# Performance work log

Hardware: AMD Instinct MI355X
Metric: run time of the kernel (lower is better)

Reference implementation:

```python
import jax, jax.numpy as jnp
import numpy as np

EPS = 0.05
T = 0.1
SINKHORN_ITERS = 3


def _l2norm(x, axis=1, eps=1e-12):
    # torch.nn.functional.normalize: x / max(||x||, eps)
    n = jnp.sqrt(jnp.sum(x * x, axis=axis, keepdims=True))
    return x / jnp.maximum(n, eps)


def _sinkhorn(sim, eps, niters):
    # SwAV-style sinkhorn. sim: [B, K]
    Q = jnp.exp(sim / eps).T            # [K, B]
    Q = Q / jnp.sum(Q)
    K, B = Q.shape

    def body(Qc, _):
        Qc = Qc / (jnp.sum(Qc, axis=1, keepdims=True) * K)  # row normalize
        Qc = Qc / (jnp.sum(Qc, axis=0, keepdims=True) * B)  # col normalize
        return Qc, None

    Q, _ = jax.lax.scan(body, Q, None, length=niters)
    return (Q * B).T                     # [B, K]


def _kl_div_logit(pred, target):
    # KLDivLoss(batchmean) on log_softmax(pred) vs target probs
    logp = jax.nn.log_softmax(pred, axis=1)
    B = pred.shape[0]
    return jnp.sum(target * (jnp.log(target) - logp)) / B


def _forward_once(c, nq, nk):
    sim = jnp.matmul(nk, c.T)                                 # [B, K]
    code = jax.lax.stop_gradient(_sinkhorn(sim, EPS, SINKHORN_ITERS))
    pred = jnp.matmul(nq, c.T) / T
    return _kl_div_logit(pred, code)


def setup_inputs() -> dict:
    key = jax.random.key(0)
    k1, k2, k3 = jax.random.split(key, 3)
    q = jax.random.normal(k1, (16384, 256), dtype=jnp.float32)
    k = jax.random.normal(k2, (16384, 256), dtype=jnp.float32)
    cluster_center = jax.random.normal(k3, (3000, 256), dtype=jnp.float32)
    return {"q": q, "k": k, "cluster_center": cluster_center}


def reference(q, k, cluster_center):
    nq = _l2norm(q, axis=1)
    nk = _l2norm(k, axis=1)
    c = _l2norm(cluster_center, axis=1)
    loss1 = _forward_once(c, nq, nk)
    loss2 = _forward_once(c, nk, nq)
    return (loss1 + loss2) / 2.0
```

## Files before the change

kernel.cpp:

```cpp
#include <hip/hip_runtime.h>

#define BATCH 16384
#define DIM   256
#define KC    3000
#define KCPAD 3072
#define NBLK  256

typedef __bf16   bf16x8  __attribute__((ext_vector_type(8)));
typedef float    floatx4 __attribute__((ext_vector_type(4)));
typedef _Float16 half8   __attribute__((ext_vector_type(8)));

#define GLD16(gptr, lptr)                                                              \
  __builtin_amdgcn_global_load_lds((const __attribute__((address_space(1))) void*)(gptr), \
                                   (__attribute__((address_space(3))) void*)(lptr), 16, 0, 0)

__device__ __forceinline__ float dpp_red_sum(float x) {
  int xi;
  xi = __builtin_amdgcn_update_dpp(0, __float_as_int(x), 0x111, 0xf, 0xf, true);
  x += __int_as_float(xi);
  xi = __builtin_amdgcn_update_dpp(0, __float_as_int(x), 0x112, 0xf, 0xf, true);
  x += __int_as_float(xi);
  xi = __builtin_amdgcn_update_dpp(0, __float_as_int(x), 0x114, 0xf, 0xf, true);
  x += __int_as_float(xi);
  xi = __builtin_amdgcn_update_dpp(0, __float_as_int(x), 0x118, 0xf, 0xf, true);
  x += __int_as_float(xi);
  xi = __builtin_amdgcn_update_dpp(0, __float_as_int(x), 0x142, 0xa, 0xf, false);
  x += __int_as_float(xi);
  xi = __builtin_amdgcn_update_dpp(0, __float_as_int(x), 0x143, 0xc, 0xf, false);
  x += __int_as_float(xi);
  return x;
}

__global__ __launch_bounds__(256) void normalize_all(const float* __restrict__ q,
                                                     const float* __restrict__ k,
                                                     const float* __restrict__ c,
                                                     __bf16* __restrict__ nq,
                                                     __bf16* __restrict__ nk,
                                                     __bf16* __restrict__ nc) {
  __shared__ float s4[4];
  int row = blockIdx.x;
  int t = threadIdx.x;
  const float* src;
  __bf16* dst;
  int srow;
  bool live;
  if (row < BATCH) {
    src = q; dst = nq; srow = row; live = true;
  } else if (row < 2 * BATCH) {
    src = k; dst = nk; srow = row - BATCH; live = true;
  } else {
    src = c; dst = nc; srow = row - 2 * BATCH; live = srow < KC;
  }
  float v = live ? src[(size_t)srow * DIM + t] : 0.f;
  float ss = dpp_red_sum(v * v);
  __syncthreads();
  if ((t & 63) == 63) s4[t >> 6] = ss;
  __syncthreads();
  float tot = s4[0] + s4[1] + s4[2] + s4[3];
  float inv = 1.f / fmaxf(sqrtf(tot), 1e-12f);
  dst[(size_t)srow * DIM + t] = (__bf16)(v * inv);
}

__global__ __launch_bounds__(256) void gemm_bf16(const __bf16* __restrict__ A,
                                                 const __bf16* __restrict__ Bm,
                                                 _Float16* __restrict__ S,
                                                 float* __restrict__ csum0) {
  __shared__ __align__(16) __bf16 As[128 * 32];
  __shared__ __align__(16) __bf16 Bs[128 * 32];
  const int tid = threadIdx.x;
  const int bm = blockIdx.x * 128;
  const int bn = blockIdx.y * 128;
  const int wid = tid >> 6;
  const int lane = tid & 63;
  const int wm = (wid >> 1) * 64;
  const int wn = (wid & 1) * 64;
  const int frow = lane & 15;
  const int fk = (lane >> 4) * 8;

  floatx4 acc[4][4] = {};

  for (int kt = 0; kt < DIM; kt += 32) {
    __syncthreads();
#pragma unroll
    for (int c = 0; c < 2; ++c) {
      int idx = tid + c * 256;
      int r = idx >> 2;
      int o = (idx & 3) * 8;
      GLD16(A + (size_t)(bm + r) * DIM + kt + o, &As[idx * 8]);
      GLD16(Bm + (size_t)(bn + r) * DIM + kt + o, &Bs[idx * 8]);
    }
    __syncthreads();
    bf16x8 af[4], bfr[4];
#pragma unroll
    for (int i = 0; i < 4; ++i)
      af[i] = *reinterpret_cast<const bf16x8*>(&As[(wm + i * 16 + frow) * 32 + fk]);
#pragma unroll
    for (int j = 0; j < 4; ++j)
      bfr[j] = *reinterpret_cast<const bf16x8*>(&Bs[(wn + j * 16 + frow) * 32 + fk]);
#pragma unroll
    for (int i = 0; i < 4; ++i)
#pragma unroll
      for (int j = 0; j < 4; ++j)
        acc[i][j] = __builtin_amdgcn_mfma_f32_16x16x32_bf16(af[i], bfr[j], acc[i][j], 0, 0, 0);
  }

  const int rgrp = (lane >> 4) * 4;
  const int cl = lane & 15;
#pragma unroll
  for (int j = 0; j < 4; ++j) {
    int colb = bn + wn + j * 16 + cl;
    bool valid = colb < KC;
    float csumj = 0.f;
#pragma unroll
    for (int i = 0; i < 4; ++i) {
#pragma unroll
      for (int r = 0; r < 4; ++r) {
        int rowb = bm + wm + i * 16 + rgrp + r;
        float sv = acc[i][j][r];
        S[(size_t)rowb * KCPAD + colb] = (_Float16)(valid ? sv : -3000.0f);
        csumj += __expf(20.f * sv);
      }
    }
    csumj = valid ? csumj : 0.f;
    csumj += __shfl_xor(csumj, 16, 64);
    csumj += __shfl_xor(csumj, 32, 64);
    if (lane < 16 && valid) atomicAdd(&csum0[colb], csumj);
  }
}

__global__ __launch_bounds__(256) void reduB(const float* __restrict__ partK,
                                             const float* __restrict__ partQ, int nparts,
                                             float* __restrict__ uK, float* __restrict__ wK,
                                             float* __restrict__ uQ, float* __restrict__ wQ) {
  int b = blockIdx.x;
  const float* parts;
  float *u, *w;
  if (b < 12) { parts = partK; u = uK; w = wK; }
  else        { parts = partQ; u = uQ; w = wQ; b -= 12; }
  int col = b * 256 + threadIdx.x;
  float s;
  if (nparts == 1) {
    s = parts[col];
  } else {
    float a0 = 0.f, a1 = 0.f, a2 = 0.f, a3 = 0.f;
    for (int i = 0; i < nparts; i += 4) {
      a0 += parts[(size_t)(i + 0) * KCPAD + col];
      a1 += parts[(size_t)(i + 1) * KCPAD + col];
      a2 += parts[(size_t)(i + 2) * KCPAD + col];
      a3 += parts[(size_t)(i + 3) * KCPAD + col];
    }
    s = (a0 + a1) + (a2 + a3);
  }
  if (col >= KC) { u[col] = 0.f; w[col] = 0.f; return; }
  float uu = 1.f / (3000.f * s);
  u[col] = uu;
  w[col] = uu * logf(uu);
}

__global__ __launch_bounds__(384, 2) void sinkp2(const _Float16* __restrict__ Sk,
                                                 const _Float16* __restrict__ Sq,
                                                 const float* __restrict__ uK,
                                                 const float* __restrict__ uQ,
                                                 float* __restrict__ partK,
                                                 float* __restrict__ partQ) {
  __shared__ float wred[16][6];
  __shared__ float vsh[16];
  const int t = threadIdx.x;
  const int w = t >> 6;
  const int lane = t & 63;
  const int col0 = t * 8;

  const _Float16* S;
  const float* uin;
  float* part;
  int rblk = blockIdx.x;
  if (rblk < NBLK) { S = Sk; uin = uK; part = partK; }
  else             { S = Sq; uin = uQ; part = partQ; rblk -= NBLK; }

  float u[8];
  {
    float4 c0 = *reinterpret_cast<const float4*>(&uin[col0]);
    float4 c1 = *reinterpret_cast<const float4*>(&uin[col0 + 4]);
    u[0] = c0.x; u[1] = c0.y; u[2] = c0.z; u[3] = c0.w;
    u[4] = c1.x; u[5] = c1.y; u[6] = c1.z; u[7] = c1.w;
  }

  const int r0 = rblk * 64;
  float creg[8] = {0.f, 0.f, 0.f, 0.f, 0.f, 0.f, 0.f, 0.f};

  for (int ch = 0; ch < 4; ++ch) {
    const int rb = r0 + ch * 16;
    half8 hv[16];
#pragma unroll
    for (int r = 0; r < 16; ++r)
      hv[r] = *reinterpret_cast<const half8*>(&S[(size_t)(rb + r) * KCPAD + col0]);

    float d[16];
#pragma unroll
    for (int r = 0; r < 16; ++r) {
      float dot = 0.f;
#pragma unroll
      for (int j = 0; j < 8; ++j) dot += __expf(20.f * (float)hv[r][j]) * u[j];
      d[r] = dot;
    }
#pragma unroll
    for (int r = 0; r < 16; ++r) d[r] = dpp_red_sum(d[r]);
    if (lane == 63) {
#pragma unroll
      for (int r = 0; r < 16; ++r) wred[r][w] = d[r];
    }
    __syncthreads();
    if (t < 16) {
      float tot = wred[t][0] + wred[t][1] + wred[t][2] + wred[t][3] + wred[t][4] + wred[t][5];
      vsh[t] = 1.f / (16384.f * tot);
    }
    __syncthreads();
#pragma unroll
    for (int r = 0; r < 16; ++r) {
      float v = vsh[r];
#pragma unroll
      for (int j = 0; j < 8; ++j) creg[j] += __expf(20.f * (float)hv[r][j]) * v;
    }
    __syncthreads();
  }

  float4* pp = reinterpret_cast<float4*>(&part[(size_t)rblk * KCPAD + col0]);
  pp[0] = make_float4(creg[0], creg[1], creg[2], creg[3]);
  pp[1] = make_float4(creg[4], creg[5], creg[6], creg[7]);
}

__global__ __launch_bounds__(384, 2) void kl_kernel(
    const _Float16* __restrict__ Sk, const _Float16* __restrict__ Sq,
    const float* __restrict__ uK, const float* __restrict__ wK,
    const float* __restrict__ uQ, const float* __restrict__ wQ,
    float* __restrict__ accOut) {
  __shared__ float wred[32][6][6];
  const int t = threadIdx.x;
  const int w = t >> 6;
  const int lane = t & 63;
  const int col0 = t * 8;

  float uk[8], wk[8], uq[8], wq[8];
  {
    float4 a0 = *reinterpret_cast<const float4*>(&uK[col0]);
    float4 a1 = *reinterpret_cast<const float4*>(&uK[col0 + 4]);
    float4 b0 = *reinterpret_cast<const float4*>(&wK[col0]);
    float4 b1 = *reinterpret_cast<const float4*>(&wK[col0 + 4]);
    float4 c0 = *reinterpret_cast<const float4*>(&uQ[col0]);
    float4 c1 = *reinterpret_cast<const float4*>(&uQ[col0 + 4]);
    float4 e0 = *reinterpret_cast<const float4*>(&wQ[col0]);
    float4 e1 = *reinterpret_cast<const float4*>(&wQ[col0 + 4]);
    uk[0]=a0.x;uk[1]=a0.y;uk[2]=a0.z;uk[3]=a0.w;uk[4]=a1.x;uk[5]=a1.y;uk[6]=a1.z;uk[7]=a1.w;
    wk[0]=b0.x;wk[1]=b0.y;wk[2]=b0.z;wk[3]=b0.w;wk[4]=b1.x;wk[5]=b1.y;wk[6]=b1.z;wk[7]=b1.w;
    uq[0]=c0.x;uq[1]=c0.y;uq[2]=c0.z;uq[3]=c0.w;uq[4]=c1.x;uq[5]=c1.y;uq[6]=c1.z;uq[7]=c1.w;
    wq[0]=e0.x;wq[1]=e0.y;wq[2]=e0.z;wq[3]=e0.w;wq[4]=e1.x;wq[5]=e1.y;wq[6]=e1.z;wq[7]=e1.w;
  }

  const int r0 = blockIdx.x * 32;
  for (int r = 0; r < 32; ++r) {
    size_t base = (size_t)(r0 + r) * KCPAD + col0;
    half8 hk = *reinterpret_cast<const half8*>(&Sk[base]);
    half8 hq = *reinterpret_cast<const half8*>(&Sq[base]);
    float Dk = 0.f, Ek = 0.f, hks = 0.f, Dq = 0.f, Eq = 0.f, hqs = 0.f;
#pragma unroll
    for (int j = 0; j < 8; ++j) {
      float sk = (float)hk[j], sq = (float)hq[j];
      float tk = __expf(10.f * sk), tq = __expf(10.f * sq);
      float ek = tk * tk, eq = tq * tq;
      hks += tk; hqs += tq;
      Dk += ek * uk[j];
      Dq += eq * uq[j];
      Ek += ek * (wk[j] + uk[j] * (20.f * sk - 10.f * sq));
      Eq += eq * (wq[j] + uq[j] * (20.f * sq - 10.f * sk));
    }
    Dk = dpp_red_sum(Dk);  Ek = dpp_red_sum(Ek);  hks = dpp_red_sum(hks);
    Dq = dpp_red_sum(Dq);  Eq = dpp_red_sum(Eq);  hqs = dpp_red_sum(hqs);
    if (lane == 63) {
      wred[r][w][0] = Dk; wred[r][w][1] = Ek; wred[r][w][2] = hks;
      wred[r][w][3] = Dq; wred[r][w][4] = Eq; wred[r][w][5] = hqs;
    }
  }
  __syncthreads();

  float contrib = 0.f;
  if (t < 32) {
    float v[6] = {0.f, 0.f, 0.f, 0.f, 0.f, 0.f};
#pragma unroll
    for (int ww = 0; ww < 6; ++ww)
#pragma unroll
      for (int qq = 0; qq < 6; ++qq) v[qq] += wred[t][ww][qq];
    contrib = logf(v[5]) - logf(v[0]) + v[1] / v[0]
            + logf(v[2]) - logf(v[3]) + v[4] / v[3];
  }
  if (w == 0) {
#pragma unroll
    for (int o = 32; o; o >>= 1) contrib += __shfl_down(contrib, o, 64);
    if (lane == 0) atomicAdd(accOut, contrib);
  }
}

__global__ void finalize_k(const float* __restrict__ acc, float* __restrict__ out) {
  out[0] = acc[0] * (1.f / 32768.f);
}

extern "C" void kernel_launch(void* const* d_in, const int* in_sizes, int n_in,
                              void* d_out, int out_size, void* d_ws, size_t ws_size,
                              hipStream_t stream) {
  const float* q = (const float*)d_in[0];
  const float* k = (const float*)d_in[1];
  const float* c = (const float*)d_in[2];
  float* out = (float*)d_out;

  char* ws = (char*)d_ws;
  float* partK = (float*)ws;
  float* partQ = (float*)(ws + 3145728);
  __bf16* nk = (__bf16*)(ws);
  __bf16* nc = (__bf16*)(ws + 8388608);
  _Float16* Sq = (_Float16*)(ws + 9961472);
  _Float16* Sk = (_Float16*)(ws + 110624768);
  __bf16* nq = (__bf16*)(ws + 110624768);
  float* fb = (float*)(ws + 211288064);
  float* csK0 = fb;
  float* csQ0 = fb + 3072;
  float* accv = fb + 6144;
  float* uK0 = fb + 6160;  float* wK0 = fb + 9232;
  float* uK1 = fb + 12304; float* wK1 = fb + 15376;
  float* uK2 = fb + 18448; float* wK2 = fb + 21520;
  float* uQ0 = fb + 24592; float* wQ0 = fb + 27664;
  float* uQ1 = fb + 30736; float* wQ1 = fb + 33808;
  float* uQ2 = fb + 36880; float* wQ2 = fb + 39952;

  hipMemsetAsync(fb, 0, 6160 * sizeof(float), stream);

  normalize_all<<<2 * BATCH + KCPAD, 256, 0, stream>>>(q, k, c, nq, nk, nc);

  dim3 gg(BATCH / 128, KCPAD / 128);
  gemm_bf16<<<gg, 256, 0, stream>>>(nq, nc, Sq, csQ0);
  gemm_bf16<<<gg, 256, 0, stream>>>(nk, nc, Sk, csK0);

  reduB<<<24, 256, 0, stream>>>(csK0, csQ0, 1, uK0, wK0, uQ0, wQ0);

  sinkp2<<<2 * NBLK, 384, 0, stream>>>(Sk, Sq, uK0, uQ0, partK, partQ);
  reduB<<<24, 256, 0, stream>>>(partK, partQ, NBLK, uK1, wK1, uQ1, wQ1);
  sinkp2<<<2 * NBLK, 384, 0, stream>>>(Sk, Sq, uK1, uQ1, partK, partQ);
  reduB<<<24, 256, 0, stream>>>(partK, partQ, NBLK, uK2, wK2, uQ2, wQ2);

  kl_kernel<<<512, 384, 0, stream>>>(Sk, Sq, uK2, wK2, uQ2, wQ2, accv);
  finalize_k<<<1, 1, 0, stream>>>(accv, out);
}
```

Before: 424.9 us.

## Swizzle GEMM LDS, prefetch sinkhorn/KL rows, wave-per-row normalize

Normalize now processes one row per wavefront with vectorized float4 loads and no shared-memory reduction. The GEMM applies an XOR swizzle to the LDS tile layout to reduce bank conflicts on fragment reads. The sinkhorn pass and the KL kernel double-buffer their row loads in registers to overlap memory latency with exp-heavy compute, and one barrier is removed. This raises register pressure and could affect occupancy.

```diff
diff --git a/kernel.cpp b/kernel.cpp
--- a/kernel.cpp
+++ b/kernel.cpp
@@ -6,6 +6,7 @@
 #define KCPAD 3072
 #define NBLK  256
 
+typedef __bf16   bf16x4  __attribute__((ext_vector_type(4)));
 typedef __bf16   bf16x8  __attribute__((ext_vector_type(8)));
 typedef float    floatx4 __attribute__((ext_vector_type(4)));
 typedef _Float16 half8   __attribute__((ext_vector_type(8)));
@@ -37,28 +38,30 @@
                                                      __bf16* __restrict__ nq,
                                                      __bf16* __restrict__ nk,
                                                      __bf16* __restrict__ nc) {
-  __shared__ float s4[4];
-  int row = blockIdx.x;
-  int t = threadIdx.x;
+  const int wid = threadIdx.x >> 6;
+  const int lane = threadIdx.x & 63;
+  int row = blockIdx.x * 4 + wid;
   const float* src;
   __bf16* dst;
   int srow;
-  bool live;
+  bool live = true;
   if (row < BATCH) {
-    src = q; dst = nq; srow = row; live = true;
+    src = q; dst = nq; srow = row;
   } else if (row < 2 * BATCH) {
-    src = k; dst = nk; srow = row - BATCH; live = true;
+    src = k; dst = nk; srow = row - BATCH;
   } else {
     src = c; dst = nc; srow = row - 2 * BATCH; live = srow < KC;
   }
-  float v = live ? src[(size_t)srow * DIM + t] : 0.f;
-  float ss = dpp_red_sum(v * v);
-  __syncthreads();
-  if ((t & 63) == 63) s4[t >> 6] = ss;
-  __syncthreads();
-  float tot = s4[0] + s4[1] + s4[2] + s4[3];
-  float inv = 1.f / fmaxf(sqrtf(tot), 1e-12f);
-  dst[(size_t)srow * DIM + t] = (__bf16)(v * inv);
+  float4 v = make_float4(0.f, 0.f, 0.f, 0.f);
+  if (live) v = *reinterpret_cast<const float4*>(&src[(size_t)srow * DIM + lane * 4]);
+  float ss = v.x * v.x + v.y * v.y + v.z * v.z + v.w * v.w;
+  ss = dpp_red_sum(ss);
+  ss = __shfl(ss, 63, 64);
+  float inv = 1.f / fmaxf(sqrtf(ss), 1e-12f);
+  bf16x4 o;
+  o[0] = (__bf16)(v.x * inv); o[1] = (__bf16)(v.y * inv);
+  o[2] = (__bf16)(v.z * inv); o[3] = (__bf16)(v.w * inv);
+  *reinterpret_cast<bf16x4*>(&dst[(size_t)srow * DIM + lane * 4]) = o;
 }
 
 __global__ __launch_bounds__(256) void gemm_bf16(const __bf16* __restrict__ A,
@@ -75,7 +78,25 @@
   const int wm = (wid >> 1) * 64;
   const int wn = (wid & 1) * 64;
   const int frow = lane & 15;
-  const int fk = (lane >> 4) * 8;
+  const int fq = lane >> 4;
+
+  int src_off[2];
+#pragma unroll
+  for (int c = 0; c < 2; ++c) {
+    int idx = tid + c * 256;
+    int r = idx >> 2;
+    int cc = idx & 3;
+    int swz = (r & 3) ^ ((r >> 2) & 3);
+    src_off[c] = r * DIM + ((cc ^ swz) << 3);
+  }
+  int a_pos[4], b_pos[4];
+#pragma unroll
+  for (int i = 0; i < 4; ++i) {
+    int rowA = wm + i * 16 + frow;
+    int rowB = wn + i * 16 + frow;
+    a_pos[i] = rowA * 32 + ((fq ^ ((rowA & 3) ^ ((rowA >> 2) & 3))) << 3);
+    b_pos[i] = rowB * 32 + ((fq ^ ((rowB & 3) ^ ((rowB >> 2) & 3))) << 3);
+  }
 
   floatx4 acc[4][4] = {};
 
@@ -84,19 +105,15 @@
 #pragma unroll
     for (int c = 0; c < 2; ++c) {
       int idx = tid + c * 256;
-      int r = idx >> 2;
-      int o = (idx & 3) * 8;
-      GLD16(A + (size_t)(bm + r) * DIM + kt + o, &As[idx * 8]);
-      GLD16(Bm + (size_t)(bn + r) * DIM + kt + o, &Bs[idx * 8]);
+      GLD16(A + (size_t)bm * DIM + kt + src_off[c], &As[idx * 8]);
+      GLD16(Bm + (size_t)bn * DIM + kt + src_off[c], &Bs[idx * 8]);
     }
     __syncthreads();
     bf16x8 af[4], bfr[4];
 #pragma unroll
-    for (int i = 0; i < 4; ++i)
-      af[i] = *reinterpret_cast<const bf16x8*>(&As[(wm + i * 16 + frow) * 32 + fk]);
-#pragma unroll
-    for (int j = 0; j < 4; ++j)
-      bfr[j] = *reinterpret_cast<const bf16x8*>(&Bs[(wn + j * 16 + frow) * 32 + fk]);
+    for (int i = 0; i < 4; ++i) af[i] = *reinterpret_cast<const bf16x8*>(&As[a_pos[i]]);
+#pragma unroll
+    for (int j = 0; j < 4; ++j) bfr[j] = *reinterpret_cast<const bf16x8*>(&Bs[b_pos[j]]);
 #pragma unroll
     for (int i = 0; i < 4; ++i)
 #pragma unroll
@@ -188,19 +205,25 @@
   const int r0 = rblk * 64;
   float creg[8] = {0.f, 0.f, 0.f, 0.f, 0.f, 0.f, 0.f, 0.f};
 
+  half8 hv[2][16];
+#pragma unroll
+  for (int r = 0; r < 16; ++r)
+    hv[0][r] = *reinterpret_cast<const half8*>(&S[(size_t)(r0 + r) * KCPAD + col0]);
+
+#pragma unroll
   for (int ch = 0; ch < 4; ++ch) {
-    const int rb = r0 + ch * 16;
-    half8 hv[16];
+    const int cur = ch & 1, nxt = cur ^ 1;
+    const int rbn = r0 + ((ch < 3) ? (ch + 1) * 16 : 0);
 #pragma unroll
     for (int r = 0; r < 16; ++r)
-      hv[r] = *reinterpret_cast<const half8*>(&S[(size_t)(rb + r) * KCPAD + col0]);
+      hv[nxt][r] = *reinterpret_cast<const half8*>(&S[(size_t)(rbn + r) * KCPAD + col0]);
 
     float d[16];
 #pragma unroll
     for (int r = 0; r < 16; ++r) {
       float dot = 0.f;
 #pragma unroll
-      for (int j = 0; j < 8; ++j) dot += __expf(20.f * (float)hv[r][j]) * u[j];
+      for (int j = 0; j < 8; ++j) dot += __expf(20.f * (float)hv[cur][r][j]) * u[j];
       d[r] = dot;
     }
 #pragma unroll
@@ -219,9 +242,8 @@
     for (int r = 0; r < 16; ++r) {
       float v = vsh[r];
 #pragma unroll
-      for (int j = 0; j < 8; ++j) creg[j] += __expf(20.f * (float)hv[r][j]) * v;
-    }
-    __syncthreads();
+      for (int j = 0; j < 8; ++j) creg[j] += __expf(20.f * (float)hv[cur][r][j]) * v;
+    }
   }
 
   float4* pp = reinterpret_cast<float4*>(&part[(size_t)rblk * KCPAD + col0]);
@@ -257,28 +279,52 @@
   }
 
   const int r0 = blockIdx.x * 32;
-  for (int r = 0; r < 32; ++r) {
-    size_t base = (size_t)(r0 + r) * KCPAD + col0;
-    half8 hk = *reinterpret_cast<const half8*>(&Sk[base]);
-    half8 hq = *reinterpret_cast<const half8*>(&Sq[base]);
-    float Dk = 0.f, Ek = 0.f, hks = 0.f, Dq = 0.f, Eq = 0.f, hqs = 0.f;
-#pragma unroll
-    for (int j = 0; j < 8; ++j) {
-      float sk = (float)hk[j], sq = (float)hq[j];
-      float tk = __expf(10.f * sk), tq = __expf(10.f * sq);
-      float ek = tk * tk, eq = tq * tq;
-      hks += tk; hqs += tq;
-      Dk += ek * uk[j];
-      Dq += eq * uq[j];
-      Ek += ek * (wk[j] + uk[j] * (20.f * sk - 10.f * sq));
-      Eq += eq * (wq[j] + uq[j] * (20.f * sq - 10.f * sk));
-    }
-    Dk = dpp_red_sum(Dk);  Ek = dpp_red_sum(Ek);  hks = dpp_red_sum(hks);
-    Dq = dpp_red_sum(Dq);  Eq = dpp_red_sum(Eq);  hqs = dpp_red_sum(hqs);
+  size_t base0 = (size_t)r0 * KCPAD + col0;
+  half8 a0 = *reinterpret_cast<const half8*>(&Sk[base0]);
+  half8 b0 = *reinterpret_cast<const half8*>(&Sq[base0]);
+  half8 a1 = *reinterpret_cast<const half8*>(&Sk[base0 + KCPAD]);
+  half8 b1 = *reinterpret_cast<const half8*>(&Sq[base0 + KCPAD]);
+
+#pragma unroll
+  for (int r = 0; r < 32; r += 2) {
+    const int rn = (r + 2 < 32) ? r + 2 : 0;
+    size_t nb = (size_t)(r0 + rn) * KCPAD + col0;
+    half8 na0 = *reinterpret_cast<const half8*>(&Sk[nb]);
+    half8 nb0 = *reinterpret_cast<const half8*>(&Sq[nb]);
+    half8 na1 = *reinterpret_cast<const half8*>(&Sk[nb + KCPAD]);
+    half8 nb1 = *reinterpret_cast<const half8*>(&Sq[nb + KCPAD]);
+
+    float P[2][6];
+#pragma unroll
+    for (int rr = 0; rr < 2; ++rr) {
+      half8 hk = rr ? a1 : a0;
+      half8 hq = rr ? b1 : b0;
+      float Dk = 0.f, Ek = 0.f, hks = 0.f, Dq = 0.f, Eq = 0.f, hqs = 0.f;
+#pragma unroll
+      for (int j = 0; j < 8; ++j) {
+        float sk = (float)hk[j], sq = (float)hq[j];
+        float tk = __expf(10.f * sk), tq = __expf(10.f * sq);
+        float ek = tk * tk, eq = tq * tq;
+        hks += tk; hqs += tq;
+        Dk += ek * uk[j];
+        Dq += eq * uq[j];
+        Ek += ek * (wk[j] + uk[j] * (20.f * sk - 10.f * sq));
+        Eq += eq * (wq[j] + uq[j] * (20.f * sq - 10.f * sk));
+      }
+      P[rr][0] = Dk; P[rr][1] = Ek; P[rr][2] = hks;
+      P[rr][3] = Dq; P[rr][4] = Eq; P[rr][5] = hqs;
+    }
+#pragma unroll
+    for (int rr = 0; rr < 2; ++rr)
+#pragma unroll
+      for (int qq = 0; qq < 6; ++qq) P[rr][qq] = dpp_red_sum(P[rr][qq]);
     if (lane == 63) {
-      wred[r][w][0] = Dk; wred[r][w][1] = Ek; wred[r][w][2] = hks;
-      wred[r][w][3] = Dq; wred[r][w][4] = Eq; wred[r][w][5] = hqs;
-    }
+#pragma unroll
+      for (int rr = 0; rr < 2; ++rr)
+#pragma unroll
+        for (int qq = 0; qq < 6; ++qq) wred[r + rr][w][qq] = P[rr][qq];
+    }
+    a0 = na0; b0 = nb0; a1 = na1; b1 = nb1;
   }
   __syncthreads();
 
@@ -332,7 +378,7 @@
 
   hipMemsetAsync(fb, 0, 6160 * sizeof(float), stream);
 
-  normalize_all<<<2 * BATCH + KCPAD, 256, 0, stream>>>(q, k, c, nq, nk, nc);
+  normalize_all<<<(2 * BATCH + KCPAD) / 4, 256, 0, stream>>>(q, k, c, nq, nk, nc);
 
   dim3 gg(BATCH / 128, KCPAD / 128);
   gemm_bf16<<<gg, 256, 0, stream>>>(nq, nc, Sq, csQ0);
```

Measured after the change: 739.8 us. 74.1% more time.
